# Performance work log

Measured on AMD Instinct MI355X. Metric: run time of the kernel, lower is better.

## Reference

```python
import jax, jax.numpy as jnp
import numpy as np

H, I, E, TOPK = 2048, 4096, 8, 2
B, S = 2, 2048

def setup_inputs() -> dict:
    key = jax.random.key(0)
    ks = jax.random.split(key, 6)
    x = jax.random.normal(ks[0], (B, S, H), dtype=jnp.float32)
    expert_indices = jax.random.randint(ks[1], (B, S, TOPK), 0, E, dtype=jnp.int64)
    expert_weights = jax.random.uniform(ks[2], (B, S, TOPK), dtype=jnp.float32)
    gate_proj = jax.random.normal(ks[3], (E, I, H), dtype=jnp.float32) * 0.02
    up_proj = jax.random.normal(ks[4], (E, I, H), dtype=jnp.float32) * 0.02
    down_proj = jax.random.normal(ks[5], (E, H, I), dtype=jnp.float32) * 0.02
    return {"x": x, "expert_indices": expert_indices, "expert_weights": expert_weights,
            "gate_proj": gate_proj, "up_proj": up_proj, "down_proj": down_proj}

def reference(x, expert_indices, expert_weights, gate_proj, up_proj, down_proj):
    b, s, h = x.shape
    T = b * s
    xf = x.reshape(T, h)                                   # [T, H]
    idx = expert_indices.reshape(T, -1)                    # [T, K]
    w = expert_weights.reshape(T, -1)                      # [T, K]
    n_exp = gate_proj.shape[0]
    # Per-token combined weight for each expert (sums duplicate slots, matching
    # the original weighted scatter-add over (token, slot) pairs).
    onehot = jax.nn.one_hot(idx, n_exp, dtype=xf.dtype)    # [T, K, E]
    we = jnp.einsum('tk,tke->et', w, onehot)               # [E, T]

    def step(acc, inp):
        g_w, u_w, d_w, w_e = inp                           # [I,H], [I,H], [H,I], [T]
        g = xf @ g_w.T                                     # [T, I]
        u = xf @ u_w.T                                     # [T, I]
        inter = g * jax.nn.sigmoid(g) * u                  # fused SiLU(g) * u
        acc = acc + w_e[:, None] * (inter @ d_w.T)         # weighted combine
        return acc, None

    out0 = jnp.zeros((T, h), dtype=x.dtype)
    out, _ = jax.lax.scan(step, out0, (gate_proj, up_proj, down_proj, we))
    return out.reshape(b, s, h)
```

## Files before the change

### kernel.cpp

```cpp
#include <hip/hip_runtime.h>
#include <hip/hip_bf16.h>
#include <stdint.h>

#define H_DIM 2048
#define I_DIM 4096
#define NEXP  8
#define NTOK  4096
#define NPAIR 8192
#define PAD_ROWS (NPAIR + 256)

#define MiB (1024ull * 1024ull)
#define WS_COUNTS   0ull
#define WS_OFFSETS  256ull
#define WS_TOKID    1024ull
#define WS_SLOT     (64ull * 1024)
#define WS_PAIRW    (128ull * 1024)
#define WS_XG       (1ull * MiB)
#define WS_INTER    (36ull * MiB)
#define WS_Y        (104ull * MiB)
#define WS_GW       (176ull * MiB)
#define WS_UW       (304ull * MiB)
#define WS_DW       (432ull * MiB)
#define WS_FULL     (560ull * MiB)

typedef __attribute__((ext_vector_type(8))) short bf16x8;
typedef __attribute__((ext_vector_type(4))) float f32x4;

#if defined(__has_builtin)
#if __has_builtin(__builtin_amdgcn_cvt_pk_bf16_f32)
#define HAVE_CVT_PK 1
#endif
#endif

__device__ __forceinline__ uint32_t bf16_bits_rne(float x) {
  uint32_t u = __float_as_uint(x);
  return (u + 0x7FFFu + ((u >> 16) & 1u)) >> 16;
}
__device__ __forceinline__ uint32_t pk_bf16(float a, float b) {
#ifdef HAVE_CVT_PK
  auto r = __builtin_amdgcn_cvt_pk_bf16_f32(a, b);
  return __builtin_bit_cast(uint32_t, r);
#else
  return bf16_bits_rne(a) | (bf16_bits_rne(b) << 16);
#endif
}
__device__ __forceinline__ uint16_t bf16_one(float x) {
  return (uint16_t)(pk_bf16(x, x) & 0xFFFFu);
}

__device__ __forceinline__ void async_load16(const void* g, void* l) {
  __builtin_amdgcn_global_load_lds(
      (const __attribute__((address_space(1))) void*)g,
      (__attribute__((address_space(3))) void*)l, 16, 0, 0);
}

#define WAIT_VM6()  do { asm volatile("s_waitcnt vmcnt(6)" ::: "memory"); __builtin_amdgcn_sched_barrier(0); } while (0)
#define WAIT_VM0()  do { asm volatile("s_waitcnt vmcnt(0)" ::: "memory"); __builtin_amdgcn_sched_barrier(0); } while (0)
#define BARRIER()   do { __builtin_amdgcn_s_barrier(); asm volatile("" ::: "memory"); } while (0)

__global__ void route_kernel(const int* __restrict__ idx, const float* __restrict__ wts,
                             int* __restrict__ ws_counts, int* __restrict__ ws_offsets,
                             int* __restrict__ tokid, int* __restrict__ slotOf,
                             float* __restrict__ pairw) {
  __shared__ int s_cnt[NEXP], s_off[NEXP], s_cur[NEXP];
  int tid = threadIdx.x;
  if (tid < NEXP) s_cnt[tid] = 0;
  __syncthreads();
  for (int p = tid; p < NPAIR; p += 256) atomicAdd(&s_cnt[idx[p]], 1);
  __syncthreads();
  if (tid == 0) {
    int acc = 0;
    for (int e = 0; e < NEXP; e++) { s_off[e] = acc; s_cur[e] = acc; acc += s_cnt[e]; }
  }
  __syncthreads();
  for (int p = tid; p < NPAIR; p += 256) {
    int e = idx[p];
    int slot = atomicAdd(&s_cur[e], 1);
    tokid[slot] = p >> 1;
    slotOf[p] = slot;
    pairw[slot] = wts[p];
  }
  if (tid < NEXP) { ws_counts[tid] = s_cnt[tid]; ws_offsets[tid] = s_off[tid]; }
}

__global__ void gather_cast_kernel(const float* __restrict__ x, const int* __restrict__ tokid,
                                   uint16_t* __restrict__ xg) {
  int p = blockIdx.x;
  int t = tokid[p];
  int c = threadIdx.x * 8;
  const float4* src = (const float4*)(x + (size_t)t * H_DIM + c);
  float4 v0 = src[0], v1 = src[1];
  uint4 o;
  o.x = pk_bf16(v0.x, v0.y); o.y = pk_bf16(v0.z, v0.w);
  o.z = pk_bf16(v1.x, v1.y); o.w = pk_bf16(v1.z, v1.w);
  *(uint4*)(xg + (size_t)p * H_DIM + c) = o;
}

__global__ void cast3_kernel(const float* __restrict__ g, const float* __restrict__ u,
                             const float* __restrict__ d,
                             uint16_t* __restrict__ gw, uint16_t* __restrict__ uw,
                             uint16_t* __restrict__ dw) {
  const float* src = blockIdx.y == 0 ? g : (blockIdx.y == 1 ? u : d);
  uint16_t*    dst = blockIdx.y == 0 ? gw : (blockIdx.y == 1 ? uw : dw);
  const long long n8 = (long long)NEXP * I_DIM * H_DIM / 8;
  long long stride = (long long)gridDim.x * blockDim.x;
  for (long long i = (long long)blockIdx.x * blockDim.x + threadIdx.x; i < n8; i += stride) {
    const float4* s = (const float4*)(src + i * 8);
    float4 a = s[0], b = s[1];
    uint4 o = { pk_bf16(a.x, a.y), pk_bf16(a.z, a.w), pk_bf16(b.x, b.y), pk_bf16(b.z, b.w) };
    *(uint4*)(dst + i * 8) = o;
  }
}

#define T1_A    (256 * 64)
#define T1_B    (64 * 64)
#define T1_ELE  (T1_A + 2 * T1_B)

__global__ __launch_bounds__(512, 1)
void gemm1_v2(const uint16_t* __restrict__ xg,
              const uint16_t* __restrict__ gw, const uint16_t* __restrict__ uw,
              const int* __restrict__ ws_counts, const int* __restrict__ ws_offsets,
              uint16_t* __restrict__ inter) {
  int e = blockIdx.z;
  int cnt = ws_counts[e];
  int rowTile = blockIdx.y;
  if (rowTile * 256 >= cnt) return;
  int off = ws_offsets[e];
  int colBase = blockIdx.x * 64;
  size_t rowBase = (size_t)off + (size_t)rowTile * 256;

  __shared__ uint16_t lds[3 * T1_ELE];

  int tid = threadIdx.x, lane = tid & 63, w = tid >> 6;
  int r8 = lane >> 3;
  int gsw = ((lane & 7) ^ r8) << 3;

  const uint16_t* srcA[4];
#pragma unroll
  for (int c = 0; c < 4; c++)
    srcA[c] = xg + (rowBase + (size_t)(w * 32 + c * 8 + r8)) * H_DIM + gsw;
  const uint16_t* srcG = gw + ((size_t)e * I_DIM + colBase + w * 8 + r8) * H_DIM + gsw;
  const uint16_t* srcU = uw + ((size_t)e * I_DIM + colBase + w * 8 + r8) * H_DIM + gsw;

  const int dA = w * 2048;
  const int dG = T1_A + w * 512;
  const int dU = T1_A + T1_B + w * 512;

  f32x4 accg[4][2], accu[4][2];
  f32x4 zero = {0.f, 0.f, 0.f, 0.f};
#pragma unroll
  for (int mi = 0; mi < 4; mi++)
#pragma unroll
    for (int ni = 0; ni < 2; ni++) { accg[mi][ni] = zero; accu[mi][ni] = zero; }

  auto STG = [&](int kt, int b) {
    uint16_t* lb = lds + b * T1_ELE;
    int ko = kt * 64;
#pragma unroll
    for (int c = 0; c < 4; c++) async_load16(srcA[c] + ko, lb + dA + c * 512);
    async_load16(srcG + ko, lb + dG);
    async_load16(srcU + ko, lb + dU);
  };

  STG(0, 0); STG(1, 1);
  WAIT_VM6();
  BARRIER();

  int wr = w >> 1, wc = w & 1;
  int wm = wr * 64, wn = wc * 32;
  int lcol = lane & 15, quad = lane >> 4;
  int sx = (lcol & 7) << 3;

  const int NT = H_DIM / 64;
  for (int t = 0; t < NT; ++t) {
    if (t + 2 < NT) STG(t + 2, (t + 2) % 3);
    const uint16_t* lb = lds + (t % 3) * T1_ELE;
#pragma unroll
    for (int ks = 0; ks < 2; ks++) {
      int krs = (ks * 32 + quad * 8) ^ sx;
      bf16x8 af[4], bg_[2], bu_[2];
#pragma unroll
      for (int mi = 0; mi < 4; mi++)
        af[mi] = *(const bf16x8*)(lb + (wm + mi * 16 + lcol) * 64 + krs);
#pragma unroll
      for (int ni = 0; ni < 2; ni++) {
        bg_[ni] = *(const bf16x8*)(lb + T1_A + (wn + ni * 16 + lcol) * 64 + krs);
        bu_[ni] = *(const bf16x8*)(lb + T1_A + T1_B + (wn + ni * 16 + lcol) * 64 + krs);
      }
      __builtin_amdgcn_s_setprio(1);
#pragma unroll
      for (int mi = 0; mi < 4; mi++)
#pragma unroll
        for (int ni = 0; ni < 2; ni++) {
          accg[mi][ni] = __builtin_amdgcn_mfma_f32_16x16x32_bf16(af[mi], bg_[ni], accg[mi][ni], 0, 0, 0);
          accu[mi][ni] = __builtin_amdgcn_mfma_f32_16x16x32_bf16(af[mi], bu_[ni], accu[mi][ni], 0, 0, 0);
        }
      __builtin_amdgcn_s_setprio(0);
    }
    if (t + 2 < NT) { WAIT_VM6(); } else { WAIT_VM0(); }
    BARRIER();
  }

  int col0 = colBase + wn;
#pragma unroll
  for (int mi = 0; mi < 4; mi++) {
#pragma unroll
    for (int r = 0; r < 4; r++) {
      int localRow = rowTile * 256 + wm + mi * 16 + quad * 4 + r;
      if (localRow < cnt) {
        size_t prow = (size_t)off + localRow;
#pragma unroll
        for (int ni = 0; ni < 2; ni++) {
          float g = accg[mi][ni][r], u = accu[mi][ni][r];
          float v = (g / (1.f + __expf(-g))) * u;
          inter[prow * I_DIM + col0 + ni * 16 + lcol] = bf16_one(v);
        }
      }
    }
  }
}

#define T2_A    (256 * 64)
#define T2_B    (128 * 64)
#define T2_ELE  (T2_A + T2_B)

__global__ __launch_bounds__(512, 1)
void gemm2_v2(const uint16_t* __restrict__ inter, const uint16_t* __restrict__ dw,
              const int* __restrict__ ws_counts, const int* __restrict__ ws_offsets,
              const float* __restrict__ pairw, float* __restrict__ y) {
  int e = blockIdx.z;
  int cnt = ws_counts[e];
  int rowTile = blockIdx.y;
  if (rowTile * 256 >= cnt) return;
  int off = ws_offsets[e];
  int colBase = blockIdx.x * 128;
  size_t rowBase = (size_t)off + (size_t)rowTile * 256;

  __shared__ uint16_t lds[3 * T2_ELE];

  int tid = threadIdx.x, lane = tid & 63, w = tid >> 6;
  int r8 = lane >> 3;
  int gsw = ((lane & 7) ^ r8) << 3;

  const uint16_t* srcA[4];
#pragma unroll
  for (int c = 0; c < 4; c++)
    srcA[c] = inter + (rowBase + (size_t)(w * 32 + c * 8 + r8)) * I_DIM + gsw;
  const uint16_t* srcB[2];
#pragma unroll
  for (int c = 0; c < 2; c++)
    srcB[c] = dw + ((size_t)e * H_DIM + colBase + w * 16 + c * 8 + r8) * I_DIM + gsw;

  const int dA = w * 2048;
  const int dB = T2_A + w * 1024;

  f32x4 acc[4][4];
  f32x4 zero = {0.f, 0.f, 0.f, 0.f};
#pragma unroll
  for (int mi = 0; mi < 4; mi++)
#pragma unroll
    for (int ni = 0; ni < 4; ni++) acc[mi][ni] = zero;

  auto STG = [&](int kt, int b) {
    uint16_t* lb = lds + b * T2_ELE;
    int ko = kt * 64;
#pragma unroll
    for (int c = 0; c < 4; c++) async_load16(srcA[c] + ko, lb + dA + c * 512);
#pragma unroll
    for (int c = 0; c < 2; c++) async_load16(srcB[c] + ko, lb + dB + c * 512);
  };

  STG(0, 0); STG(1, 1);
  WAIT_VM6();
  BARRIER();

  int wr = w >> 1, wc = w & 1;
  int wm = wr * 64, wn = wc * 64;
  int lcol = lane & 15, quad = lane >> 4;
  int sx = (lcol & 7) << 3;

  const int NT = I_DIM / 64;
  for (int t = 0; t < NT; ++t) {
    if (t + 2 < NT) STG(t + 2, (t + 2) % 3);
    const uint16_t* lb = lds + (t % 3) * T2_ELE;
#pragma unroll
    for (int ks = 0; ks < 2; ks++) {
      int krs = (ks * 32 + quad * 8) ^ sx;
      bf16x8 af[4], bf_[4];
#pragma unroll
      for (int mi = 0; mi < 4; mi++)
        af[mi] = *(const bf16x8*)(lb + (wm + mi * 16 + lcol) * 64 + krs);
#pragma unroll
      for (int ni = 0; ni < 4; ni++)
        bf_[ni] = *(const bf16x8*)(lb + T2_A + (wn + ni * 16 + lcol) * 64 + krs);
      __builtin_amdgcn_s_setprio(1);
#pragma unroll
      for (int mi = 0; mi < 4; mi++)
#pragma unroll
        for (int ni = 0; ni < 4; ni++)
          acc[mi][ni] = __builtin_amdgcn_mfma_f32_16x16x32_bf16(af[mi], bf_[ni], acc[mi][ni], 0, 0, 0);
      __builtin_amdgcn_s_setprio(0);
    }
    if (t + 2 < NT) { WAIT_VM6(); } else { WAIT_VM0(); }
    BARRIER();
  }

  int col0 = colBase + wn;
#pragma unroll
  for (int mi = 0; mi < 4; mi++) {
#pragma unroll
    for (int r = 0; r < 4; r++) {
      int localRow = rowTile * 256 + wm + mi * 16 + quad * 4 + r;
      if (localRow < cnt) {
        size_t prow = (size_t)off + localRow;
        float wgt = pairw[prow];
        float* yr = y + prow * H_DIM + col0;
#pragma unroll
        for (int ni = 0; ni < 4; ni++)
          yr[ni * 16 + lcol] = acc[mi][ni][r] * wgt;
      }
    }
  }
}

__global__ void combine_kernel(const float* __restrict__ y, const int* __restrict__ slotOf,
                               float* __restrict__ out) {
  int t = blockIdx.x;
  int s0 = slotOf[2 * t], s1 = slotOf[2 * t + 1];
  int c = threadIdx.x * 8;
  const float4* a = (const float4*)(y + (size_t)s0 * H_DIM + c);
  const float4* b = (const float4*)(y + (size_t)s1 * H_DIM + c);
  float4 a0 = a[0], a1 = a[1], b0 = b[0], b1 = b[1];
  float4 o0 = {a0.x + b0.x, a0.y + b0.y, a0.z + b0.z, a0.w + b0.w};
  float4 o1 = {a1.x + b1.x, a1.y + b1.y, a1.z + b1.z, a1.w + b1.w};
  float4* dst = (float4*)(out + (size_t)t * H_DIM + c);
  dst[0] = o0; dst[1] = o1;
}

extern "C" void kernel_launch(void* const* d_in, const int* in_sizes, int n_in,
                              void* d_out, int out_size, void* d_ws, size_t ws_size,
                              hipStream_t stream) {
  const float* x    = (const float*)d_in[0];
  const int*   eidx = (const int*)d_in[1];
  const float* ew   = (const float*)d_in[2];
  const float* gate = (const float*)d_in[3];
  const float* up   = (const float*)d_in[4];
  const float* down = (const float*)d_in[5];
  float* out = (float*)d_out;
  char* ws = (char*)d_ws;

  if (ws_size < WS_FULL) {
    hipMemsetAsync(d_out, 0, (size_t)NTOK * H_DIM * sizeof(float), stream);
    return;
  }

  int*      counts  = (int*)(ws + WS_COUNTS);
  int*      offsets = (int*)(ws + WS_OFFSETS);
  int*      tokid   = (int*)(ws + WS_TOKID);
  int*      slotOf  = (int*)(ws + WS_SLOT);
  float*    pairw   = (float*)(ws + WS_PAIRW);
  uint16_t* xg      = (uint16_t*)(ws + WS_XG);
  uint16_t* inter   = (uint16_t*)(ws + WS_INTER);
  float*    y       = (float*)(ws + WS_Y);
  uint16_t* gw      = (uint16_t*)(ws + WS_GW);
  uint16_t* uw      = (uint16_t*)(ws + WS_UW);
  uint16_t* dwp     = (uint16_t*)(ws + WS_DW);

  route_kernel<<<1, 256, 0, stream>>>(eidx, ew, counts, offsets, tokid, slotOf, pairw);
  gather_cast_kernel<<<NPAIR, 256, 0, stream>>>(x, tokid, xg);
  cast3_kernel<<<dim3(2048, 3), 256, 0, stream>>>(gate, up, down, gw, uw, dwp);

  gemm1_v2<<<dim3(I_DIM / 64, NPAIR / 256, NEXP), 512, 0, stream>>>(
      xg, gw, uw, counts, offsets, inter);
  gemm2_v2<<<dim3(H_DIM / 128, NPAIR / 256, NEXP), 512, 0, stream>>>(
      inter, dwp, counts, offsets, pairw, y);
  combine_kernel<<<NTOK, 256, 0, stream>>>(y, slotOf, out);
}
```

Measured before the change: 1.333 ms.

## Restructure MoE GEMMs with half-K double buffering and wider gate/up tiles

```diff
diff --git a/kernel.cpp b/kernel.cpp
--- a/kernel.cpp
+++ b/kernel.cpp
@@ -54,6 +54,7 @@
       (__attribute__((address_space(3))) void*)l, 16, 0, 0);
 }
 
+#define WAIT_VM8()  do { asm volatile("s_waitcnt vmcnt(8)" ::: "memory"); __builtin_amdgcn_sched_barrier(0); } while (0)
 #define WAIT_VM6()  do { asm volatile("s_waitcnt vmcnt(6)" ::: "memory"); __builtin_amdgcn_sched_barrier(0); } while (0)
 #define WAIT_VM0()  do { asm volatile("s_waitcnt vmcnt(0)" ::: "memory"); __builtin_amdgcn_sched_barrier(0); } while (0)
 #define BARRIER()   do { __builtin_amdgcn_s_barrier(); asm volatile("" ::: "memory"); } while (0)
@@ -112,12 +113,10 @@
   }
 }
 
-#define T1_A    (256 * 64)
-#define T1_B    (64 * 64)
-#define T1_ELE  (T1_A + 2 * T1_B)
-
-__global__ __launch_bounds__(512, 1)
-void gemm1_v2(const uint16_t* __restrict__ xg,
+#define NT1 (H_DIM / 64)
+
+__global__ __launch_bounds__(512, 2)
+void gemm1_v3(const uint16_t* __restrict__ xg,
               const uint16_t* __restrict__ gw, const uint16_t* __restrict__ uw,
               const int* __restrict__ ws_counts, const int* __restrict__ ws_offsets,
               uint16_t* __restrict__ inter) {
@@ -126,106 +125,123 @@
   int rowTile = blockIdx.y;
   if (rowTile * 256 >= cnt) return;
   int off = ws_offsets[e];
-  int colBase = blockIdx.x * 64;
+  int colBase = blockIdx.x * 128;
   size_t rowBase = (size_t)off + (size_t)rowTile * 256;
 
-  __shared__ uint16_t lds[3 * T1_ELE];
+  __shared__ uint16_t sA[2][2][256][32];
+  __shared__ uint16_t sB[2][2][256][32];
 
   int tid = threadIdx.x, lane = tid & 63, w = tid >> 6;
-  int r8 = lane >> 3;
-  int gsw = ((lane & 7) ^ r8) << 3;
-
-  const uint16_t* srcA[4];
-#pragma unroll
-  for (int c = 0; c < 4; c++)
-    srcA[c] = xg + (rowBase + (size_t)(w * 32 + c * 8 + r8)) * H_DIM + gsw;
-  const uint16_t* srcG = gw + ((size_t)e * I_DIM + colBase + w * 8 + r8) * H_DIM + gsw;
-  const uint16_t* srcU = uw + ((size_t)e * I_DIM + colBase + w * 8 + r8) * H_DIM + gsw;
-
-  const int dA = w * 2048;
-  const int dG = T1_A + w * 512;
-  const int dU = T1_A + T1_B + w * 512;
-
-  f32x4 accg[4][2], accu[4][2];
+  int lcol = lane & 15, quad = lane >> 4;
+  int wr = w >> 2, wc = w & 3;
+
+  int lr = lane >> 2, lk = (lane & 3) * 8;
+  const uint16_t* aSrc[2];
+  const uint16_t* bSrc[2];
+#pragma unroll
+  for (int c = 0; c < 2; c++) {
+    int ar = (w * 2 + c) * 16 + lr;
+    aSrc[c] = xg + (rowBase + ar) * H_DIM + lk;
+    int jn = ar;
+    int jw = jn >> 6, v = jn & 63;
+    const uint16_t* wbase = (v < 32) ? gw : uw;
+    bSrc[c] = wbase + ((size_t)e * I_DIM + colBase + jw * 32 + (v & 31)) * H_DIM + lk;
+  }
+
+  f32x4 acc[8][4];
   f32x4 zero = {0.f, 0.f, 0.f, 0.f};
 #pragma unroll
-  for (int mi = 0; mi < 4; mi++)
-#pragma unroll
-    for (int ni = 0; ni < 2; ni++) { accg[mi][ni] = zero; accu[mi][ni] = zero; }
-
-  auto STG = [&](int kt, int b) {
-    uint16_t* lb = lds + b * T1_ELE;
-    int ko = kt * 64;
-#pragma unroll
-    for (int c = 0; c < 4; c++) async_load16(srcA[c] + ko, lb + dA + c * 512);
-    async_load16(srcG + ko, lb + dG);
-    async_load16(srcU + ko, lb + dU);
+  for (int mf = 0; mf < 8; mf++)
+#pragma unroll
+    for (int ni = 0; ni < 4; ni++) acc[mf][ni] = zero;
+
+  auto STG_A = [&](int buf, int kh, int kt) {
+    int ko = kt * 64 + kh * 32;
+    async_load16(aSrc[0] + ko, &sA[buf][kh][(w * 2 + 0) * 16][0]);
+    async_load16(aSrc[1] + ko, &sA[buf][kh][(w * 2 + 1) * 16][0]);
   };
-
-  STG(0, 0); STG(1, 1);
-  WAIT_VM6();
+  auto STG_B = [&](int buf, int kh, int kt) {
+    int ko = kt * 64 + kh * 32;
+    async_load16(bSrc[0] + ko, &sB[buf][kh][(w * 2 + 0) * 16][0]);
+    async_load16(bSrc[1] + ko, &sB[buf][kh][(w * 2 + 1) * 16][0]);
+  };
+
+#define RD1(KS, MQ)                                                                   \
+  _Pragma("unroll") for (int mi = 0; mi < 4; mi++)                                    \
+    af[mi] = *(const bf16x8*)&sA[b][KS][wr * 128 + MQ * 64 + mi * 16 + lcol][quad * 8]; \
+  _Pragma("unroll") for (int ni = 0; ni < 4; ni++)                                    \
+    bb[ni] = *(const bf16x8*)&sB[b][KS][wc * 64 + ni * 16 + lcol][quad * 8];
+
+#define MM1(MQ)                                                                       \
+  __builtin_amdgcn_s_setprio(1);                                                      \
+  _Pragma("unroll") for (int mi = 0; mi < 4; mi++)                                    \
+    _Pragma("unroll") for (int ni = 0; ni < 4; ni++)                                  \
+      acc[MQ * 4 + mi][ni] = __builtin_amdgcn_mfma_f32_16x16x32_bf16(                 \
+          af[mi], bb[ni], acc[MQ * 4 + mi][ni], 0, 0, 0);                             \
+  __builtin_amdgcn_s_setprio(0);
+
+  STG_A(0, 0, 0); STG_B(0, 0, 0);
+  STG_A(0, 1, 0); STG_B(0, 1, 0);
+  STG_A(1, 0, 1); STG_B(1, 0, 1);
+  WAIT_VM8();
   BARRIER();
 
-  int wr = w >> 1, wc = w & 1;
-  int wm = wr * 64, wn = wc * 32;
-  int lcol = lane & 15, quad = lane >> 4;
-  int sx = (lcol & 7) << 3;
-
-  const int NT = H_DIM / 64;
-  for (int t = 0; t < NT; ++t) {
-    if (t + 2 < NT) STG(t + 2, (t + 2) % 3);
-    const uint16_t* lb = lds + (t % 3) * T1_ELE;
-#pragma unroll
-    for (int ks = 0; ks < 2; ks++) {
-      int krs = (ks * 32 + quad * 8) ^ sx;
-      bf16x8 af[4], bg_[2], bu_[2];
-#pragma unroll
-      for (int mi = 0; mi < 4; mi++)
-        af[mi] = *(const bf16x8*)(lb + (wm + mi * 16 + lcol) * 64 + krs);
-#pragma unroll
-      for (int ni = 0; ni < 2; ni++) {
-        bg_[ni] = *(const bf16x8*)(lb + T1_A + (wn + ni * 16 + lcol) * 64 + krs);
-        bu_[ni] = *(const bf16x8*)(lb + T1_A + T1_B + (wn + ni * 16 + lcol) * 64 + krs);
-      }
-      __builtin_amdgcn_s_setprio(1);
-#pragma unroll
-      for (int mi = 0; mi < 4; mi++)
-#pragma unroll
-        for (int ni = 0; ni < 2; ni++) {
-          accg[mi][ni] = __builtin_amdgcn_mfma_f32_16x16x32_bf16(af[mi], bg_[ni], accg[mi][ni], 0, 0, 0);
-          accu[mi][ni] = __builtin_amdgcn_mfma_f32_16x16x32_bf16(af[mi], bu_[ni], accu[mi][ni], 0, 0, 0);
-        }
-      __builtin_amdgcn_s_setprio(0);
-    }
-    if (t + 2 < NT) { WAIT_VM6(); } else { WAIT_VM0(); }
-    BARRIER();
-  }
-
-  int col0 = colBase + wn;
-#pragma unroll
-  for (int mi = 0; mi < 4; mi++) {
-#pragma unroll
-    for (int r = 0; r < 4; r++) {
-      int localRow = rowTile * 256 + wm + mi * 16 + quad * 4 + r;
-      if (localRow < cnt) {
-        size_t prow = (size_t)off + localRow;
-#pragma unroll
-        for (int ni = 0; ni < 2; ni++) {
-          float g = accg[mi][ni][r], u = accu[mi][ni][r];
-          float v = (g / (1.f + __expf(-g))) * u;
-          inter[prow * I_DIM + col0 + ni * 16 + lcol] = bf16_one(v);
+  for (int t = 0; t < NT1; ++t) {
+    const int b = t & 1, bn = b ^ 1;
+    const bool tail = (t >= NT1 - 2);
+    bf16x8 af[4], bb[4];
+    RD1(0, 0);
+    if (t + 1 < NT1) STG_A(bn, 1, t + 1);
+    BARRIER();
+    MM1(0);
+    BARRIER();
+    RD1(0, 1);
+    if (t + 1 < NT1) STG_B(bn, 1, t + 1);
+    BARRIER();
+    MM1(1);
+    if (tail) { WAIT_VM0(); } else { WAIT_VM8(); }
+    BARRIER();
+    RD1(1, 0);
+    if (t + 2 < NT1) STG_A(b, 0, t + 2);
+    BARRIER();
+    MM1(0);
+    BARRIER();
+    RD1(1, 1);
+    if (t + 2 < NT1) STG_B(b, 0, t + 2);
+    BARRIER();
+    MM1(1);
+    if (tail) { WAIT_VM0(); } else { WAIT_VM8(); }
+    BARRIER();
+  }
+#undef RD1
+#undef MM1
+
+#pragma unroll
+  for (int mq = 0; mq < 2; mq++) {
+#pragma unroll
+    for (int mi = 0; mi < 4; mi++) {
+#pragma unroll
+      for (int r = 0; r < 4; r++) {
+        int localRow = rowTile * 256 + wr * 128 + mq * 64 + mi * 16 + quad * 4 + r;
+        if (localRow < cnt) {
+          size_t prow = (size_t)off + localRow;
+#pragma unroll
+          for (int ni = 0; ni < 2; ni++) {
+            float g = acc[mq * 4 + mi][ni][r];
+            float u = acc[mq * 4 + mi][ni + 2][r];
+            float v = (g / (1.f + __expf(-g))) * u;
+            inter[prow * I_DIM + colBase + wc * 32 + ni * 16 + lcol] = bf16_one(v);
+          }
         }
       }
     }
   }
 }
 
-#define T2_A    (256 * 64)
-#define T2_B    (128 * 64)
-#define T2_ELE  (T2_A + T2_B)
-
-__global__ __launch_bounds__(512, 1)
-void gemm2_v2(const uint16_t* __restrict__ inter, const uint16_t* __restrict__ dw,
+#define NT2 (I_DIM / 64)
+
+__global__ __launch_bounds__(512, 2)
+void gemm2_v3(const uint16_t* __restrict__ inter, const uint16_t* __restrict__ dw,
               const int* __restrict__ ws_counts, const int* __restrict__ ws_offsets,
               const float* __restrict__ pairw, float* __restrict__ y) {
   int e = blockIdx.z;
@@ -236,23 +252,21 @@
   int colBase = blockIdx.x * 128;
   size_t rowBase = (size_t)off + (size_t)rowTile * 256;
 
-  __shared__ uint16_t lds[3 * T2_ELE];
+  __shared__ uint16_t sA[2][2][256][32];
+  __shared__ uint16_t sB[2][2][128][32];
 
   int tid = threadIdx.x, lane = tid & 63, w = tid >> 6;
-  int r8 = lane >> 3;
-  int gsw = ((lane & 7) ^ r8) << 3;
-
-  const uint16_t* srcA[4];
-#pragma unroll
-  for (int c = 0; c < 4; c++)
-    srcA[c] = inter + (rowBase + (size_t)(w * 32 + c * 8 + r8)) * I_DIM + gsw;
-  const uint16_t* srcB[2];
-#pragma unroll
-  for (int c = 0; c < 2; c++)
-    srcB[c] = dw + ((size_t)e * H_DIM + colBase + w * 16 + c * 8 + r8) * I_DIM + gsw;
-
-  const int dA = w * 2048;
-  const int dB = T2_A + w * 1024;
+  int lcol = lane & 15, quad = lane >> 4;
+  int wr = w >> 1, wc = w & 1;
+
+  int lr = lane >> 2, lk = (lane & 3) * 8;
+  const uint16_t* aSrc[2];
+#pragma unroll
+  for (int c = 0; c < 2; c++) {
+    int ar = (w * 2 + c) * 16 + lr;
+    aSrc[c] = inter + (rowBase + ar) * I_DIM + lk;
+  }
+  const uint16_t* bSrc = dw + ((size_t)e * H_DIM + colBase + w * 16 + lr) * I_DIM + lk;
 
   f32x4 acc[4][4];
   f32x4 zero = {0.f, 0.f, 0.f, 0.f};
@@ -261,60 +275,65 @@
 #pragma unroll
     for (int ni = 0; ni < 4; ni++) acc[mi][ni] = zero;
 
-  auto STG = [&](int kt, int b) {
-    uint16_t* lb = lds + b * T2_ELE;
-    int ko = kt * 64;
-#pragma unroll
-    for (int c = 0; c < 4; c++) async_load16(srcA[c] + ko, lb + dA + c * 512);
-#pragma unroll
-    for (int c = 0; c < 2; c++) async_load16(srcB[c] + ko, lb + dB + c * 512);
+  auto STG_A = [&](int buf, int kh, int kt) {
+    int ko = kt * 64 + kh * 32;
+    async_load16(aSrc[0] + ko, &sA[buf][kh][(w * 2 + 0) * 16][0]);
+    async_load16(aSrc[1] + ko, &sA[buf][kh][(w * 2 + 1) * 16][0]);
   };
-
-  STG(0, 0); STG(1, 1);
+  auto STG_B = [&](int buf, int kh, int kt) {
+    int ko = kt * 64 + kh * 32;
+    async_load16(bSrc + ko, &sB[buf][kh][w * 16][0]);
+  };
+
+#define RD2(KS)                                                                       \
+  _Pragma("unroll") for (int mi = 0; mi < 4; mi++)                                    \
+    af[mi] = *(const bf16x8*)&sA[b][KS][wr * 64 + mi * 16 + lcol][quad * 8];          \
+  _Pragma("unroll") for (int ni = 0; ni < 4; ni++)                                    \
+    bb[ni] = *(const bf16x8*)&sB[b][KS][wc * 64 + ni * 16 + lcol][quad * 8];
+
+#define MM2()                                                                         \
+  __builtin_amdgcn_s_setprio(1);                                                      \
+  _Pragma("unroll") for (int mi = 0; mi < 4; mi++)                                    \
+    _Pragma("unroll") for (int ni = 0; ni < 4; ni++)                                  \
+      acc[mi][ni] = __builtin_amdgcn_mfma_f32_16x16x32_bf16(                          \
+          af[mi], bb[ni], acc[mi][ni], 0, 0, 0);                                      \
+  __builtin_amdgcn_s_setprio(0);
+
+  STG_A(0, 0, 0); STG_B(0, 0, 0);
+  STG_A(0, 1, 0); STG_B(0, 1, 0);
+  STG_A(1, 0, 1); STG_B(1, 0, 1);
   WAIT_VM6();
   BARRIER();
 
-  int wr = w >> 1, wc = w & 1;
-  int wm = wr * 64, wn = wc * 64;
-  int lcol = lane & 15, quad = lane >> 4;
-  int sx = (lcol & 7) << 3;
-
-  const int NT = I_DIM / 64;
-  for (int t = 0; t < NT; ++t) {
-    if (t + 2 < NT) STG(t + 2, (t + 2) % 3);
-    const uint16_t* lb = lds + (t % 3) * T2_ELE;
-#pragma unroll
-    for (int ks = 0; ks < 2; ks++) {
-      int krs = (ks * 32 + quad * 8) ^ sx;
-      bf16x8 af[4], bf_[4];
-#pragma unroll
-      for (int mi = 0; mi < 4; mi++)
-        af[mi] = *(const bf16x8*)(lb + (wm + mi * 16 + lcol) * 64 + krs);
-#pragma unroll
-      for (int ni = 0; ni < 4; ni++)
-        bf_[ni] = *(const bf16x8*)(lb + T2_A + (wn + ni * 16 + lcol) * 64 + krs);
-      __builtin_amdgcn_s_setprio(1);
-#pragma unroll
-      for (int mi = 0; mi < 4; mi++)
-#pragma unroll
-        for (int ni = 0; ni < 4; ni++)
-          acc[mi][ni] = __builtin_amdgcn_mfma_f32_16x16x32_bf16(af[mi], bf_[ni], acc[mi][ni], 0, 0, 0);
-      __builtin_amdgcn_s_setprio(0);
-    }
-    if (t + 2 < NT) { WAIT_VM6(); } else { WAIT_VM0(); }
-    BARRIER();
-  }
-
-  int col0 = colBase + wn;
+  for (int t = 0; t < NT2; ++t) {
+    const int b = t & 1, bn = b ^ 1;
+    const bool tail = (t >= NT2 - 2);
+    bf16x8 af[4], bb[4];
+    RD2(0);
+    if (t + 1 < NT2) { STG_A(bn, 1, t + 1); STG_B(bn, 1, t + 1); }
+    BARRIER();
+    MM2();
+    if (tail) { WAIT_VM0(); } else { WAIT_VM6(); }
+    BARRIER();
+    RD2(1);
+    if (t + 2 < NT2) { STG_A(b, 0, t + 2); STG_B(b, 0, t + 2); }
+    BARRIER();
+    MM2();
+    if (tail) { WAIT_VM0(); } else { WAIT_VM6(); }
+    BARRIER();
+  }
+#undef RD2
+#undef MM2
+
 #pragma unroll
   for (int mi = 0; mi < 4; mi++) {
 #pragma unroll
     for (int r = 0; r < 4; r++) {
-      int localRow = rowTile * 256 + wm + mi * 16 + quad * 4 + r;
+      int localRow = rowTile * 256 + wr * 64 + mi * 16 + quad * 4 + r;
       if (localRow < cnt) {
         size_t prow = (size_t)off + localRow;
         float wgt = pairw[prow];
-        float* yr = y + prow * H_DIM + col0;
+        float* yr = y + prow * H_DIM + colBase + wc * 64;
 #pragma unroll
         for (int ni = 0; ni < 4; ni++)
           yr[ni * 16 + lcol] = acc[mi][ni][r] * wgt;
@@ -370,9 +389,9 @@
   gather_cast_kernel<<<NPAIR, 256, 0, stream>>>(x, tokid, xg);
   cast3_kernel<<<dim3(2048, 3), 256, 0, stream>>>(gate, up, down, gw, uw, dwp);
 
-  gemm1_v2<<<dim3(I_DIM / 64, NPAIR / 256, NEXP), 512, 0, stream>>>(
+  gemm1_v3<<<dim3(I_DIM / 128, NPAIR / 256, NEXP), 512, 0, stream>>>(
       xg, gw, uw, counts, offsets, inter);
-  gemm2_v2<<<dim3(H_DIM / 128, NPAIR / 256, NEXP), 512, 0, stream>>>(
+  gemm2_v3<<<dim3(H_DIM / 128, NPAIR / 256, NEXP), 512, 0, stream>>>(
       inter, dwp, counts, offsets, pairw, y);
   combine_kernel<<<NTOK, 256, 0, stream>>>(y, slotOf, out);
 }
```

New measurement: 1.525 ms. 1.14x slower.

## Fuse fp32-to-bf16 weight conversion into expert GEMM tile loads

Applied to the files above, without the earlier changes.

```diff
diff --git a/kernel.cpp b/kernel.cpp
--- a/kernel.cpp
+++ b/kernel.cpp
@@ -18,10 +18,7 @@
 #define WS_XG       (1ull * MiB)
 #define WS_INTER    (36ull * MiB)
 #define WS_Y        (104ull * MiB)
-#define WS_GW       (176ull * MiB)
-#define WS_UW       (304ull * MiB)
-#define WS_DW       (432ull * MiB)
-#define WS_FULL     (560ull * MiB)
+#define WS_FULL     (172ull * MiB)
 
 typedef __attribute__((ext_vector_type(8))) short bf16x8;
 typedef __attribute__((ext_vector_type(4))) float f32x4;
@@ -54,9 +51,11 @@
       (__attribute__((address_space(3))) void*)l, 16, 0, 0);
 }
 
-#define WAIT_VM6()  do { asm volatile("s_waitcnt vmcnt(6)" ::: "memory"); __builtin_amdgcn_sched_barrier(0); } while (0)
-#define WAIT_VM0()  do { asm volatile("s_waitcnt vmcnt(0)" ::: "memory"); __builtin_amdgcn_sched_barrier(0); } while (0)
-#define BARRIER()   do { __builtin_amdgcn_s_barrier(); asm volatile("" ::: "memory"); } while (0)
+#define WAIT_VM4()   do { asm volatile("s_waitcnt vmcnt(4)" ::: "memory"); __builtin_amdgcn_sched_barrier(0); } while (0)
+#define WAIT_VM0()   do { asm volatile("s_waitcnt vmcnt(0)" ::: "memory"); __builtin_amdgcn_sched_barrier(0); } while (0)
+#define WAIT_LGKM0() do { asm volatile("s_waitcnt lgkmcnt(0)" ::: "memory"); __builtin_amdgcn_sched_barrier(0); } while (0)
+#define BARRIER()    do { __builtin_amdgcn_s_barrier(); asm volatile("" ::: "memory"); } while (0)
+#define SBAR0()      __builtin_amdgcn_sched_barrier(0)
 
 __global__ void route_kernel(const int* __restrict__ idx, const float* __restrict__ wts,
                              int* __restrict__ ws_counts, int* __restrict__ ws_offsets,
@@ -96,29 +95,14 @@
   *(uint4*)(xg + (size_t)p * H_DIM + c) = o;
 }
 
-__global__ void cast3_kernel(const float* __restrict__ g, const float* __restrict__ u,
-                             const float* __restrict__ d,
-                             uint16_t* __restrict__ gw, uint16_t* __restrict__ uw,
-                             uint16_t* __restrict__ dw) {
-  const float* src = blockIdx.y == 0 ? g : (blockIdx.y == 1 ? u : d);
-  uint16_t*    dst = blockIdx.y == 0 ? gw : (blockIdx.y == 1 ? uw : dw);
-  const long long n8 = (long long)NEXP * I_DIM * H_DIM / 8;
-  long long stride = (long long)gridDim.x * blockDim.x;
-  for (long long i = (long long)blockIdx.x * blockDim.x + threadIdx.x; i < n8; i += stride) {
-    const float4* s = (const float4*)(src + i * 8);
-    float4 a = s[0], b = s[1];
-    uint4 o = { pk_bf16(a.x, a.y), pk_bf16(a.z, a.w), pk_bf16(b.x, b.y), pk_bf16(b.z, b.w) };
-    *(uint4*)(dst + i * 8) = o;
-  }
-}
-
-#define T1_A    (256 * 64)
-#define T1_B    (64 * 64)
-#define T1_ELE  (T1_A + 2 * T1_B)
+#define NT1 (H_DIM / 64)
+#define T1_ELE  (256 * 64 + 2 * 64 * 64)
+#define BG_OFF  (256 * 64)
+#define BU_OFF  (256 * 64 + 64 * 64)
 
 __global__ __launch_bounds__(512, 1)
-void gemm1_v2(const uint16_t* __restrict__ xg,
-              const uint16_t* __restrict__ gw, const uint16_t* __restrict__ uw,
+void gemm1_v4(const uint16_t* __restrict__ xg,
+              const float* __restrict__ gate, const float* __restrict__ up,
               const int* __restrict__ ws_counts, const int* __restrict__ ws_offsets,
               uint16_t* __restrict__ inter) {
   int e = blockIdx.z;
@@ -132,74 +116,116 @@
   __shared__ uint16_t lds[3 * T1_ELE];
 
   int tid = threadIdx.x, lane = tid & 63, w = tid >> 6;
-  int r8 = lane >> 3;
-  int gsw = ((lane & 7) ^ r8) << 3;
-
-  const uint16_t* srcA[4];
+  int r8 = lane >> 3, g8 = lane & 7;
+  int gsw = (g8 ^ r8) << 3;
+
+  const uint16_t* aSrc[4];
 #pragma unroll
   for (int c = 0; c < 4; c++)
-    srcA[c] = xg + (rowBase + (size_t)(w * 32 + c * 8 + r8)) * H_DIM + gsw;
-  const uint16_t* srcG = gw + ((size_t)e * I_DIM + colBase + w * 8 + r8) * H_DIM + gsw;
-  const uint16_t* srcU = uw + ((size_t)e * I_DIM + colBase + w * 8 + r8) * H_DIM + gsw;
-
-  const int dA = w * 2048;
-  const int dG = T1_A + w * 512;
-  const int dU = T1_A + T1_B + w * 512;
-
-  f32x4 accg[4][2], accu[4][2];
-  f32x4 zero = {0.f, 0.f, 0.f, 0.f};
-#pragma unroll
-  for (int mi = 0; mi < 4; mi++)
-#pragma unroll
-    for (int ni = 0; ni < 2; ni++) { accg[mi][ni] = zero; accu[mi][ni] = zero; }
-
-  auto STG = [&](int kt, int b) {
-    uint16_t* lb = lds + b * T1_ELE;
-    int ko = kt * 64;
-#pragma unroll
-    for (int c = 0; c < 4; c++) async_load16(srcA[c] + ko, lb + dA + c * 512);
-    async_load16(srcG + ko, lb + dG);
-    async_load16(srcU + ko, lb + dU);
-  };
-
-  STG(0, 0); STG(1, 1);
-  WAIT_VM6();
-  BARRIER();
+    aSrc[c] = xg + (rowBase + (size_t)(w * 32 + c * 8 + r8)) * H_DIM + gsw;
+
+  const float* gSrc = gate + ((size_t)e * I_DIM + colBase + w * 8 + r8) * H_DIM + g8 * 8;
+  const float* uSrc = up   + ((size_t)e * I_DIM + colBase + w * 8 + r8) * H_DIM + g8 * 8;
+  const int bgWr = BG_OFF + (w * 8 + r8) * 64 + ((g8 ^ r8) << 3);
+  const int buWr = BU_OFF + (w * 8 + r8) * 64 + ((g8 ^ r8) << 3);
 
   int wr = w >> 1, wc = w & 1;
   int wm = wr * 64, wn = wc * 32;
   int lcol = lane & 15, quad = lane >> 4;
   int sx = (lcol & 7) << 3;
 
-  const int NT = H_DIM / 64;
-  for (int t = 0; t < NT; ++t) {
-    if (t + 2 < NT) STG(t + 2, (t + 2) % 3);
-    const uint16_t* lb = lds + (t % 3) * T1_ELE;
-#pragma unroll
-    for (int ks = 0; ks < 2; ks++) {
-      int krs = (ks * 32 + quad * 8) ^ sx;
-      bf16x8 af[4], bg_[2], bu_[2];
-#pragma unroll
-      for (int mi = 0; mi < 4; mi++)
-        af[mi] = *(const bf16x8*)(lb + (wm + mi * 16 + lcol) * 64 + krs);
-#pragma unroll
-      for (int ni = 0; ni < 2; ni++) {
-        bg_[ni] = *(const bf16x8*)(lb + T1_A + (wn + ni * 16 + lcol) * 64 + krs);
-        bu_[ni] = *(const bf16x8*)(lb + T1_A + T1_B + (wn + ni * 16 + lcol) * 64 + krs);
-      }
-      __builtin_amdgcn_s_setprio(1);
-#pragma unroll
-      for (int mi = 0; mi < 4; mi++)
-#pragma unroll
-        for (int ni = 0; ni < 2; ni++) {
-          accg[mi][ni] = __builtin_amdgcn_mfma_f32_16x16x32_bf16(af[mi], bg_[ni], accg[mi][ni], 0, 0, 0);
-          accu[mi][ni] = __builtin_amdgcn_mfma_f32_16x16x32_bf16(af[mi], bu_[ni], accu[mi][ni], 0, 0, 0);
-        }
-      __builtin_amdgcn_s_setprio(0);
-    }
-    if (t + 2 < NT) { WAIT_VM6(); } else { WAIT_VM0(); }
+  f32x4 accg[4][2], accu[4][2];
+  f32x4 zero = {0.f, 0.f, 0.f, 0.f};
+#pragma unroll
+  for (int mi = 0; mi < 4; mi++)
+#pragma unroll
+    for (int ni = 0; ni < 2; ni++) { accg[mi][ni] = zero; accu[mi][ni] = zero; }
+
+#define COMP1(LB) do {                                                                 \
+    _Pragma("unroll")                                                                  \
+    for (int ks = 0; ks < 2; ks++) {                                                   \
+      const int krs = (ks * 32 + quad * 8) ^ sx;                                       \
+      bf16x8 af[4], bgf[2], buf_[2];                                                   \
+      _Pragma("unroll") for (int mi = 0; mi < 4; mi++)                                 \
+        af[mi] = *(const bf16x8*)((LB) + (wm + mi * 16 + lcol) * 64 + krs);            \
+      _Pragma("unroll") for (int ni = 0; ni < 2; ni++) {                               \
+        bgf[ni]  = *(const bf16x8*)((LB) + BG_OFF + (wn + ni * 16 + lcol) * 64 + krs); \
+        buf_[ni] = *(const bf16x8*)((LB) + BU_OFF + (wn + ni * 16 + lcol) * 64 + krs); \
+      }                                                                                \
+      __builtin_amdgcn_s_setprio(1);                                                   \
+      _Pragma("unroll") for (int mi = 0; mi < 4; mi++)                                 \
+        _Pragma("unroll") for (int ni = 0; ni < 2; ni++) {                             \
+          accg[mi][ni] = __builtin_amdgcn_mfma_f32_16x16x32_bf16(af[mi], bgf[ni],      \
+                                                                 accg[mi][ni], 0, 0, 0);\
+          accu[mi][ni] = __builtin_amdgcn_mfma_f32_16x16x32_bf16(af[mi], buf_[ni],     \
+                                                                 accu[mi][ni], 0, 0, 0);\
+        }                                                                              \
+      __builtin_amdgcn_s_setprio(0);                                                   \
+    }                                                                                  \
+  } while (0)
+
+#define ITER1(T, B0) do {                                                              \
+    const int t_ = (T);                                                                \
+    uint16_t* lb  = lds + (B0) * T1_ELE;                                               \
+    uint16_t* lbn = lds + (((B0) + 1) % 3) * T1_ELE;                                   \
+    uint16_t* lb2 = lds + (((B0) + 2) % 3) * T1_ELE;                                   \
+    float4 g0, g1, u0, u1;                                                             \
+    const bool hasB = (t_ + 1 < NT1);                                                  \
+    if (hasB) {                                                                        \
+      const float4* gp = (const float4*)(gSrc + (size_t)(t_ + 1) * 64);                \
+      g0 = gp[0]; g1 = gp[1];                                                          \
+      const float4* upp = (const float4*)(uSrc + (size_t)(t_ + 1) * 64);               \
+      u0 = upp[0]; u1 = upp[1];                                                        \
+    }                                                                                  \
+    SBAR0();                                                                           \
+    if (t_ + 2 < NT1) {                                                                \
+      const int ko = (t_ + 2) * 64;                                                    \
+      async_load16(aSrc[0] + ko, lb2 + w * 2048 + 0 * 512);                            \
+      async_load16(aSrc[1] + ko, lb2 + w * 2048 + 1 * 512);                            \
+      async_load16(aSrc[2] + ko, lb2 + w * 2048 + 2 * 512);                            \
+      async_load16(aSrc[3] + ko, lb2 + w * 2048 + 3 * 512);                            \
+    }                                                                                  \
+    SBAR0();                                                                           \
+    COMP1(lb);                                                                         \
+    if (t_ + 2 < NT1) { WAIT_VM4(); } else { WAIT_VM0(); }                             \
+    if (hasB) {                                                                        \
+      uint4 og = { pk_bf16(g0.x, g0.y), pk_bf16(g0.z, g0.w),                           \
+                   pk_bf16(g1.x, g1.y), pk_bf16(g1.z, g1.w) };                         \
+      uint4 ou = { pk_bf16(u0.x, u0.y), pk_bf16(u0.z, u0.w),                           \
+                   pk_bf16(u1.x, u1.y), pk_bf16(u1.z, u1.w) };                         \
+      *(uint4*)(lbn + bgWr) = og;                                                      \
+      *(uint4*)(lbn + buWr) = ou;                                                      \
+      WAIT_LGKM0();                                                                    \
+    }                                                                                  \
+    BARRIER();                                                                         \
+  } while (0)
+
+  {
+#pragma unroll
+    for (int c = 0; c < 4; c++) async_load16(aSrc[c], lds + w * 2048 + c * 512);
+    SBAR0();
+    const float4* gp = (const float4*)gSrc;
+    float4 g0 = gp[0], g1 = gp[1];
+    const float4* upp = (const float4*)uSrc;
+    float4 u0 = upp[0], u1 = upp[1];
+    SBAR0();
+#pragma unroll
+    for (int c = 0; c < 4; c++) async_load16(aSrc[c] + 64, lds + T1_ELE + w * 2048 + c * 512);
+    WAIT_VM4();
+    uint4 og = { pk_bf16(g0.x, g0.y), pk_bf16(g0.z, g0.w),
+                 pk_bf16(g1.x, g1.y), pk_bf16(g1.z, g1.w) };
+    uint4 ou = { pk_bf16(u0.x, u0.y), pk_bf16(u0.z, u0.w),
+                 pk_bf16(u1.x, u1.y), pk_bf16(u1.z, u1.w) };
+    *(uint4*)(lds + bgWr) = og;
+    *(uint4*)(lds + buWr) = ou;
+    WAIT_LGKM0();
     BARRIER();
   }
+
+  for (int t = 0; t < 30; t += 3) { ITER1(t, 0); ITER1(t + 1, 1); ITER1(t + 2, 2); }
+  ITER1(30, 0); ITER1(31, 1);
+#undef ITER1
+#undef COMP1
 
   int col0 = colBase + wn;
 #pragma unroll
@@ -220,12 +246,12 @@
   }
 }
 
-#define T2_A    (256 * 64)
-#define T2_B    (128 * 64)
-#define T2_ELE  (T2_A + T2_B)
+#define NT2 (I_DIM / 64)
+#define T2_ELE  (256 * 64 + 128 * 64)
+#define BD_OFF  (256 * 64)
 
 __global__ __launch_bounds__(512, 1)
-void gemm2_v2(const uint16_t* __restrict__ inter, const uint16_t* __restrict__ dw,
+void gemm2_v4(const uint16_t* __restrict__ inter, const float* __restrict__ down,
               const int* __restrict__ ws_counts, const int* __restrict__ ws_offsets,
               const float* __restrict__ pairw, float* __restrict__ y) {
   int e = blockIdx.z;
@@ -239,71 +265,111 @@
   __shared__ uint16_t lds[3 * T2_ELE];
 
   int tid = threadIdx.x, lane = tid & 63, w = tid >> 6;
-  int r8 = lane >> 3;
-  int gsw = ((lane & 7) ^ r8) << 3;
-
-  const uint16_t* srcA[4];
+  int r8 = lane >> 3, g8 = lane & 7;
+  int gsw = (g8 ^ r8) << 3;
+
+  const uint16_t* aSrc[4];
 #pragma unroll
   for (int c = 0; c < 4; c++)
-    srcA[c] = inter + (rowBase + (size_t)(w * 32 + c * 8 + r8)) * I_DIM + gsw;
-  const uint16_t* srcB[2];
-#pragma unroll
-  for (int c = 0; c < 2; c++)
-    srcB[c] = dw + ((size_t)e * H_DIM + colBase + w * 16 + c * 8 + r8) * I_DIM + gsw;
-
-  const int dA = w * 2048;
-  const int dB = T2_A + w * 1024;
-
-  f32x4 acc[4][4];
-  f32x4 zero = {0.f, 0.f, 0.f, 0.f};
-#pragma unroll
-  for (int mi = 0; mi < 4; mi++)
-#pragma unroll
-    for (int ni = 0; ni < 4; ni++) acc[mi][ni] = zero;
-
-  auto STG = [&](int kt, int b) {
-    uint16_t* lb = lds + b * T2_ELE;
-    int ko = kt * 64;
-#pragma unroll
-    for (int c = 0; c < 4; c++) async_load16(srcA[c] + ko, lb + dA + c * 512);
-#pragma unroll
-    for (int c = 0; c < 2; c++) async_load16(srcB[c] + ko, lb + dB + c * 512);
-  };
-
-  STG(0, 0); STG(1, 1);
-  WAIT_VM6();
-  BARRIER();
+    aSrc[c] = inter + (rowBase + (size_t)(w * 32 + c * 8 + r8)) * I_DIM + gsw;
+
+  const float* dSrc0 = down + ((size_t)e * H_DIM + colBase + w * 16 + 0 + r8) * I_DIM + g8 * 8;
+  const float* dSrc1 = down + ((size_t)e * H_DIM + colBase + w * 16 + 8 + r8) * I_DIM + g8 * 8;
+  const int bdWr0 = BD_OFF + (w * 16 + 0 + r8) * 64 + ((g8 ^ r8) << 3);
+  const int bdWr1 = BD_OFF + (w * 16 + 8 + r8) * 64 + ((g8 ^ r8) << 3);
 
   int wr = w >> 1, wc = w & 1;
   int wm = wr * 64, wn = wc * 64;
   int lcol = lane & 15, quad = lane >> 4;
   int sx = (lcol & 7) << 3;
 
-  const int NT = I_DIM / 64;
-  for (int t = 0; t < NT; ++t) {
-    if (t + 2 < NT) STG(t + 2, (t + 2) % 3);
-    const uint16_t* lb = lds + (t % 3) * T2_ELE;
-#pragma unroll
-    for (int ks = 0; ks < 2; ks++) {
-      int krs = (ks * 32 + quad * 8) ^ sx;
-      bf16x8 af[4], bf_[4];
-#pragma unroll
-      for (int mi = 0; mi < 4; mi++)
-        af[mi] = *(const bf16x8*)(lb + (wm + mi * 16 + lcol) * 64 + krs);
-#pragma unroll
-      for (int ni = 0; ni < 4; ni++)
-        bf_[ni] = *(const bf16x8*)(lb + T2_A + (wn + ni * 16 + lcol) * 64 + krs);
-      __builtin_amdgcn_s_setprio(1);
-#pragma unroll
-      for (int mi = 0; mi < 4; mi++)
-#pragma unroll
-        for (int ni = 0; ni < 4; ni++)
-          acc[mi][ni] = __builtin_amdgcn_mfma_f32_16x16x32_bf16(af[mi], bf_[ni], acc[mi][ni], 0, 0, 0);
-      __builtin_amdgcn_s_setprio(0);
-    }
-    if (t + 2 < NT) { WAIT_VM6(); } else { WAIT_VM0(); }
+  f32x4 acc[4][4];
+  f32x4 zero = {0.f, 0.f, 0.f, 0.f};
+#pragma unroll
+  for (int mi = 0; mi < 4; mi++)
+#pragma unroll
+    for (int ni = 0; ni < 4; ni++) acc[mi][ni] = zero;
+
+#define COMP2(LB) do {                                                                 \
+    _Pragma("unroll")                                                                  \
+    for (int ks = 0; ks < 2; ks++) {                                                   \
+      const int krs = (ks * 32 + quad * 8) ^ sx;                                       \
+      bf16x8 af[4], bb[4];                                                             \
+      _Pragma("unroll") for (int mi = 0; mi < 4; mi++)                                 \
+        af[mi] = *(const bf16x8*)((LB) + (wm + mi * 16 + lcol) * 64 + krs);            \
+      _Pragma("unroll") for (int ni = 0; ni < 4; ni++)                                 \
+        bb[ni] = *(const bf16x8*)((LB) + BD_OFF + (wn + ni * 16 + lcol) * 64 + krs);   \
+      __builtin_amdgcn_s_setprio(1);                                                   \
+      _Pragma("unroll") for (int mi = 0; mi < 4; mi++)                                 \
+        _Pragma("unroll") for (int ni = 0; ni < 4; ni++)                               \
+          acc[mi][ni] = __builtin_amdgcn_mfma_f32_16x16x32_bf16(af[mi], bb[ni],        \
+                                                                acc[mi][ni], 0, 0, 0); \
+      __builtin_amdgcn_s_setprio(0);                                                   \
+    }                                                                                  \
+  } while (0)
+
+#define ITER2(T, B0) do {                                                              \
+    const int t_ = (T);                                                                \
+    uint16_t* lb  = lds + (B0) * T2_ELE;                                               \
+    uint16_t* lbn = lds + (((B0) + 1) % 3) * T2_ELE;                                   \
+    uint16_t* lb2 = lds + (((B0) + 2) % 3) * T2_ELE;                                   \
+    float4 d00, d01, d10, d11;                                                         \
+    const bool hasB = (t_ + 1 < NT2);                                                  \
+    if (hasB) {                                                                        \
+      const float4* p0 = (const float4*)(dSrc0 + (size_t)(t_ + 1) * 64);               \
+      d00 = p0[0]; d01 = p0[1];                                                        \
+      const float4* p1 = (const float4*)(dSrc1 + (size_t)(t_ + 1) * 64);               \
+      d10 = p1[0]; d11 = p1[1];                                                        \
+    }                                                                                  \
+    SBAR0();                                                                           \
+    if (t_ + 2 < NT2) {                                                                \
+      const int ko = (t_ + 2) * 64;                                                    \
+      async_load16(aSrc[0] + ko, lb2 + w * 2048 + 0 * 512);                            \
+      async_load16(aSrc[1] + ko, lb2 + w * 2048 + 1 * 512);                            \
+      async_load16(aSrc[2] + ko, lb2 + w * 2048 + 2 * 512);                            \
+      async_load16(aSrc[3] + ko, lb2 + w * 2048 + 3 * 512);                            \
+    }                                                                                  \
+    SBAR0();                                                                           \
+    COMP2(lb);                                                                         \
+    if (t_ + 2 < NT2) { WAIT_VM4(); } else { WAIT_VM0(); }                             \
+    if (hasB) {                                                                        \
+      uint4 o0 = { pk_bf16(d00.x, d00.y), pk_bf16(d00.z, d00.w),                       \
+                   pk_bf16(d01.x, d01.y), pk_bf16(d01.z, d01.w) };                     \
+      uint4 o1 = { pk_bf16(d10.x, d10.y), pk_bf16(d10.z, d10.w),                       \
+                   pk_bf16(d11.x, d11.y), pk_bf16(d11.z, d11.w) };                     \
+      *(uint4*)(lbn + bdWr0) = o0;                                                     \
+      *(uint4*)(lbn + bdWr1) = o1;                                                     \
+      WAIT_LGKM0();                                                                    \
+    }                                                                                  \
+    BARRIER();                                                                         \
+  } while (0)
+
+  {
+#pragma unroll
+    for (int c = 0; c < 4; c++) async_load16(aSrc[c], lds + w * 2048 + c * 512);
+    SBAR0();
+    const float4* p0 = (const float4*)dSrc0;
+    float4 d00 = p0[0], d01 = p0[1];
+    const float4* p1 = (const float4*)dSrc1;
+    float4 d10 = p1[0], d11 = p1[1];
+    SBAR0();
+#pragma unroll
+    for (int c = 0; c < 4; c++) async_load16(aSrc[c] + 64, lds + T2_ELE + w * 2048 + c * 512);
+    WAIT_VM4();
+    uint4 o0 = { pk_bf16(d00.x, d00.y), pk_bf16(d00.z, d00.w),
+                 pk_bf16(d01.x, d01.y), pk_bf16(d01.z, d01.w) };
+    uint4 o1 = { pk_bf16(d10.x, d10.y), pk_bf16(d10.z, d10.w),
+                 pk_bf16(d11.x, d11.y), pk_bf16(d11.z, d11.w) };
+    *(uint4*)(lds + bdWr0) = o0;
+    *(uint4*)(lds + bdWr1) = o1;
+    WAIT_LGKM0();
     BARRIER();
   }
+
+  for (int t = 0; t < 60; t += 3) { ITER2(t, 0); ITER2(t + 1, 1); ITER2(t + 2, 2); }
+  ITER2(60, 0); ITER2(61, 1); ITER2(62, 2); ITER2(63, 0);
+#undef ITER2
+#undef COMP2
 
   int col0 = colBase + wn;
 #pragma unroll
@@ -362,17 +428,13 @@
   uint16_t* xg      = (uint16_t*)(ws + WS_XG);
   uint16_t* inter   = (uint16_t*)(ws + WS_INTER);
   float*    y       = (float*)(ws + WS_Y);
-  uint16_t* gw      = (uint16_t*)(ws + WS_GW);
-  uint16_t* uw      = (uint16_t*)(ws + WS_UW);
-  uint16_t* dwp     = (uint16_t*)(ws + WS_DW);
 
   route_kernel<<<1, 256, 0, stream>>>(eidx, ew, counts, offsets, tokid, slotOf, pairw);
   gather_cast_kernel<<<NPAIR, 256, 0, stream>>>(x, tokid, xg);
-  cast3_kernel<<<dim3(2048, 3), 256, 0, stream>>>(gate, up, down, gw, uw, dwp);
-
-  gemm1_v2<<<dim3(I_DIM / 64, NPAIR / 256, NEXP), 512, 0, stream>>>(
-      xg, gw, uw, counts, offsets, inter);
-  gemm2_v2<<<dim3(H_DIM / 128, NPAIR / 256, NEXP), 512, 0, stream>>>(
-      inter, dwp, counts, offsets, pairw, y);
+
+  gemm1_v4<<<dim3(I_DIM / 64, NPAIR / 256, NEXP), 512, 0, stream>>>(
+      xg, gate, up, counts, offsets, inter);
+  gemm2_v4<<<dim3(H_DIM / 128, NPAIR / 256, NEXP), 512, 0, stream>>>(
+      inter, down, counts, offsets, pairw, y);
   combine_kernel<<<NTOK, 256, 0, stream>>>(y, slotOf, out);
 }
```

After: 1.362 ms. 2.2% more time.
